# Optimization experiments

Hardware: AMD Instinct MI355X
Metric: run time of the kernel (lower is better)

## Reference

```python
import jax, jax.numpy as jnp
import numpy as np

EPS = 1e-5
THRESH = 1.5


def _compute_one(x, g_w, g_b, phi_w, phi_b, W_w, W_b, gamma, beta):
    # x: (c, w, h, z) -- single sample (torch code calls compute_x with batch 1)
    c, w, h, z = x.shape
    nz = z // 2
    # AdaptiveAvgPool3d(1) on x.permute(0,4,2,3,1): mean over (w, h, c) per z-slice -> (z,)
    p = x.mean(axis=(0, 1, 2))
    xp = x * p[None, None, None, :]
    # 1x1x1 conv projections (note: self.theta is defined but unused in the original)
    g_x = jnp.einsum('ic,cwhz->iwhz', g_w, x) + g_b[:, None, None, None]
    phi_x = jnp.einsum('ic,cwhz->iwhz', phi_w, xp) + phi_b[:, None, None, None]
    # MaxPool3d kernel (1,1,2): non-overlapping max pairs along z
    g_x = g_x.reshape(-1, w, h, nz, 2).max(axis=-1)      # (ic, w, h, nz)
    phi_x = phi_x.reshape(-1, w, h, nz, 2).max(axis=-1)  # (ic, w, h, nz)
    # theta_x: (x*p).permute(0,2,3,4,1).view(w*h, z, c)
    theta = xp.transpose(1, 2, 3, 0).reshape(w * h, z, c)
    # phi: permute(0,2,3,1,4).view(w*h, ic, nz)
    phi_m = phi_x.transpose(1, 2, 0, 3).reshape(w * h, -1, nz)
    # g: permute(0,2,3,4,1).view(w*h, nz, ic)
    g_m = g_x.transpose(1, 2, 3, 0).reshape(w * h, nz, -1)
    f = jnp.einsum('bzc,bcn->bzn', theta, phi_m)          # (wh, z, nz)
    a = jax.nn.softmax(f, axis=-1)
    y = jnp.einsum('bzn,bni->bzi', a, g_m)                # (wh, z, ic)
    y = y.reshape(w, h, z, -1).transpose(3, 0, 1, 2)      # (ic, w, h, z)
    wy = jnp.einsum('ci,iwhz->cwhz', W_w, y) + W_b[:, None, None, None]
    # BatchNorm3d in training mode on a single-sample batch: per-channel stats over (w,h,z)
    mu = wy.mean(axis=(1, 2, 3), keepdims=True)
    var = wy.var(axis=(1, 2, 3), keepdims=True)
    wy = (wy - mu) * jax.lax.rsqrt(var + EPS)
    wy = wy * gamma[:, None, None, None] + beta[:, None, None, None]
    return wy + x


def setup_inputs() -> dict:
    key = jax.random.key(0)
    ks = jax.random.split(key, 10)
    b, c, w, h, z = 2, 64, 64, 64, 64
    ic = c  # inter_channels defaults to in_channels
    x = jax.random.normal(ks[0], (b, c, w, h, z), dtype=jnp.float32)
    # spacings in [0, 3): some samples fall above spacing_thresh=1.5 (identity branch)
    spacings = jax.random.uniform(ks[1], (b, 3), dtype=jnp.float32) * 3.0
    g_w = jax.random.normal(ks[2], (ic, c), dtype=jnp.float32) * 0.1
    g_b = jax.random.normal(ks[3], (ic,), dtype=jnp.float32) * 0.1
    phi_w = jax.random.normal(ks[4], (ic, c), dtype=jnp.float32) * 0.1
    phi_b = jax.random.normal(ks[5], (ic,), dtype=jnp.float32) * 0.1
    W_w = jax.random.normal(ks[6], (c, ic), dtype=jnp.float32) * 0.1
    W_b = jax.random.normal(ks[7], (c,), dtype=jnp.float32) * 0.1
    gamma = jax.random.normal(ks[8], (c,), dtype=jnp.float32) * 0.1
    beta = jax.random.normal(ks[9], (c,), dtype=jnp.float32) * 0.1
    return {"x": x, "spacings": spacings, "g_w": g_w, "g_b": g_b,
            "phi_w": phi_w, "phi_b": phi_b, "W_w": W_w, "W_b": W_b,
            "gamma": gamma, "beta": beta}


def reference(x, spacings, g_w, g_b, phi_w, phi_b, W_w, W_b, gamma, beta):
    out = jax.vmap(_compute_one, in_axes=(0,) + (None,) * 8)(
        x, g_w, g_b, phi_w, phi_b, W_w, W_b, gamma, beta)
    use = (spacings[:, -1] <= THRESH)[:, None, None, None, None]
    return jnp.where(use, out, x)
```

## Files before the change

kernel.cpp:

```cpp
#include <hip/hip_runtime.h>
#include <hip/hip_bf16.h>
#include <math.h>

#define THRESH_SP 1.5f
#define WHZc   262144
#define CWHZc  16777216

#define WS_PSUM   0
#define WS_SLOT   128
#define WS_ZERO_N 8320
#define WS_W16_BYTE  65536
#define WS_WY_BYTE   131072
#define WS_W16_NEED  (WS_W16_BYTE + 3u*4096u*2u)
#define WS_WY_NEED   (WS_WY_BYTE + 2u*CWHZc*2u)

typedef __attribute__((ext_vector_type(8))) short bf16x8;
typedef __attribute__((ext_vector_type(4))) float floatx4;
typedef __attribute__((ext_vector_type(4))) float f32x4;
typedef __attribute__((ext_vector_type(2))) unsigned int u32x2;

#define MFMA(a, b, c) __builtin_amdgcn_mfma_f32_16x16x32_bf16((a), (b), (c), 0, 0, 0)

__device__ __forceinline__ unsigned short f2b(float f) {
    __hip_bfloat16 h = __float2bfloat16(f);
    return __builtin_bit_cast(unsigned short, h);
}
__device__ __forceinline__ float b2f(unsigned short h) {
    unsigned int u = ((unsigned int)h) << 16;
    return __builtin_bit_cast(float, u);
}
__device__ __forceinline__ bf16x8 ldfrag(const unsigned short* p, int elem_off) {
    return *(const bf16x8*)(p + elem_off);
}

__global__ __launch_bounds__(256) void k_prep(const float* __restrict__ gw,
                                              const float* __restrict__ pw,
                                              const float* __restrict__ Ww,
                                              float* __restrict__ ws,
                                              unsigned short* __restrict__ w16,
                                              int usew16) {
    const int i = blockIdx.x * 256 + threadIdx.x;
    if (i < WS_ZERO_N) ws[i] = 0.0f;
    if (usew16 && i < 4096) {
        w16[i]        = f2b(gw[i]);
        w16[4096 + i] = f2b(pw[i]);
        w16[8192 + i] = f2b(Ww[i]);
    }
}

__global__ __launch_bounds__(256) void k_pmean(const float* __restrict__ x,
                                               const float* __restrict__ sp,
                                               float* __restrict__ ws) {
    const int b = blockIdx.x >> 9;
    if (sp[b*3 + 2] > THRESH_SP) return;
    const int jb = blockIdx.x & 511;
    __shared__ float s[64];
    const int t = threadIdx.x;
    if (t < 64) s[t] = 0.0f;
    __syncthreads();
    const int idx4 = jb * 256 + t;
    const int z0 = (idx4 & 15) * 4;
    float a0 = 0.f, a1 = 0.f, a2 = 0.f, a3 = 0.f;
    const float* xb = x + (size_t)b * CWHZc;
#pragma unroll 4
    for (int it = 0; it < 32; ++it) {
        const float4 v = *(const float4*)&xb[(size_t)(idx4 + it * 131072) * 4];
        a0 += v.x; a1 += v.y; a2 += v.z; a3 += v.w;
    }
    a0 += __shfl_xor(a0, 16); a0 += __shfl_xor(a0, 32);
    a1 += __shfl_xor(a1, 16); a1 += __shfl_xor(a1, 32);
    a2 += __shfl_xor(a2, 16); a2 += __shfl_xor(a2, 32);
    a3 += __shfl_xor(a3, 16); a3 += __shfl_xor(a3, 32);
    if ((t & 63) < 16) {
        unsafeAtomicAdd(&s[z0 + 0], a0);
        unsafeAtomicAdd(&s[z0 + 1], a1);
        unsafeAtomicAdd(&s[z0 + 2], a2);
        unsafeAtomicAdd(&s[z0 + 3], a3);
    }
    __syncthreads();
    if (t < 64) unsafeAtomicAdd(&ws[WS_PSUM + b * 64 + t], s[t]);
}

#define L_WG     0
#define L_WP     9216
#define L_XA     18432
#define L_GPA    27648
#define L_PHA    32768
#define L_XB     37376
#define L_GPB    46592
#define L_PHB    51712
#define L_ATB    56320
#define L_BIAS   61440
#define L_PS     62208
#define L_TOTAL  62464

__global__ __launch_bounds__(512, 4) void k_main(
    const float* __restrict__ x, const float* __restrict__ sp,
    const float* __restrict__ gw, const float* __restrict__ gb,
    const float* __restrict__ pw, const float* __restrict__ pb,
    const float* __restrict__ Wwp, const float* __restrict__ Wbp,
    float* __restrict__ out, unsigned short* __restrict__ wy16, int use16,
    const unsigned short* __restrict__ w16, int usew16,
    float* __restrict__ ws) {
    const int blk = blockIdx.x;
    const int b = blk >> 11;
    if (sp[b*3 + 2] > THRESH_SP) return;
    const int whpair = (blk & 2047) * 2;

    __shared__ char smem[L_TOTAL];
    unsigned short* wg   = (unsigned short*)(smem + L_WG);
    unsigned short* wp   = (unsigned short*)(smem + L_WP);
    float*          bias = (float*)(smem + L_BIAS);
    float*          p_s  = (float*)(smem + L_PS);
    float*          statsf = (float*)(smem + L_PHA);

    const int t   = threadIdx.x;
    const int wv  = t >> 6;
    const int cid = wv >> 2;
    const int tt  = t & 255;
    const int l   = t & 63;
    const int lr  = l & 15;
    const int lq  = l >> 4;
    const int zt  = (wv & 3) << 4;

    unsigned short* xT   = (unsigned short*)(smem + (cid ? L_XB  : L_XA));
    unsigned short* gpT  = (unsigned short*)(smem + (cid ? L_GPB : L_GPA));
    unsigned short* phpN = (unsigned short*)(smem + (cid ? L_PHB : L_PHA));
    unsigned short* aT   = (unsigned short*)(smem + (cid ? L_ATB : L_WG));

    const int wh    = whpair + cid;
    const int xbase = b * CWHZc + wh * 64;

    {
        const int pr = tt >> 3;
        const int zo = tt & 7;
        const int c0 = pr * 2;
        const float* xc = &x[xbase + c0 * WHZc];
        const float4 A0 = *(const float4*)&xc[zo * 4];
        const float4 A1 = *(const float4*)&xc[zo * 4 + 32];
        const float4 B0 = *(const float4*)&xc[WHZc + zo * 4];
        const float4 B1 = *(const float4*)&xc[WHZc + zo * 4 + 32];
#pragma unroll
        for (int g = 0; g < 2; ++g) {
            const float4 va = g ? A1 : A0;
            const float4 vb = g ? B1 : B0;
            const int zb = (zo + 8 * g) * 4;
            const float av[4] = {va.x, va.y, va.z, va.w};
            const float bw[4] = {vb.x, vb.y, vb.z, vb.w};
#pragma unroll
            for (int j = 0; j < 4; ++j) {
                const int z = zb + j;
                const int chunk = (c0 >> 3) ^ ((z >> 2) & 3);
                const unsigned int pk =
                    (unsigned)f2b(av[j]) | ((unsigned)f2b(bw[j]) << 16);
                *(unsigned int*)&xT[z * 72 + chunk * 8 + (c0 & 7)] = pk;
            }
        }
    }
    if (usew16) {
#pragma unroll
        for (int k = 0; k < 2; ++k) {
            const int f = t + (k << 9);
            const int mat = f >> 9;
            const int i = (f & 511) >> 3, seg = f & 7;
            unsigned short* dst = mat ? wp : wg;
            *(uint4*)&dst[i*72 + seg*8] = *(const uint4*)&w16[mat*4096 + i*64 + seg*8];
        }
    } else {
#pragma unroll
        for (int k = 0; k < 4; ++k) {
            const int f = t + (k << 9);
            const int mat = f >> 10, ff = f & 1023;
            const int i = ff >> 4, c4 = ff & 15;
            const float* src = mat ? pw : gw;
            unsigned short* dst = mat ? wp : wg;
            const float4 v = *(const float4*)&src[i*64 + c4*4];
            uint2 pk;
            pk.x = (unsigned)f2b(v.x) | ((unsigned)f2b(v.y) << 16);
            pk.y = (unsigned)f2b(v.z) | ((unsigned)f2b(v.w) << 16);
            *(uint2*)&dst[i*72 + c4*4] = pk;
        }
    }
    if (t < 192) bias[t] = (t < 64) ? gb[t] : (t < 128) ? pb[t - 64] : Wbp[t - 128];
    if (t < 64)  p_s[t] = ws[WS_PSUM + b*64 + t] * (1.0f / 262144.0f);
    __syncthreads();

    const int zrow  = zt + lr;
    const int abase = zrow * 72 + ((lq ^ ((zrow >> 2) & 3)) << 3);
    const bf16x8 a0 = ldfrag(xT, abase);
    const bf16x8 a1 = ldfrag(xT, abase + 32);
    const float pz0 = p_s[zt + lq*4 + 0], pz1 = p_s[zt + lq*4 + 1];
    const float pz2 = p_s[zt + lq*4 + 2], pz3 = p_s[zt + lq*4 + 3];

    {
        const int n0 = (zt >> 1) + lq*2;
#pragma unroll
        for (int ti = 0; ti < 4; ++ti) {
            const int i = ti*16 + lr;
            const float bv = bias[i];
            floatx4 acc = {bv, bv, bv, bv};
            acc = MFMA(a0, ldfrag(wg, i*72 + lq*8), acc);
            acc = MFMA(a1, ldfrag(wg, i*72 + lq*8 + 32), acc);
            unsigned int pk = (unsigned)f2b(fmaxf(acc[0], acc[1])) |
                              ((unsigned)f2b(fmaxf(acc[2], acc[3])) << 16);
            *(unsigned int*)&gpT[i*40 + n0] = pk;
        }
    }
    __syncthreads();

    {
        const int n0 = (zt >> 1) + lq*2;
#pragma unroll
        for (int ti = 0; ti < 4; ++ti) {
            const int i = ti*16 + lr;
            floatx4 acc = {0.f, 0.f, 0.f, 0.f};
            acc = MFMA(a0, ldfrag(wp, i*72 + lq*8), acc);
            acc = MFMA(a1, ldfrag(wp, i*72 + lq*8 + 32), acc);
            const float bv = bias[64 + i];
            const float v0 = fmaf(acc[0], pz0, bv), v1 = fmaf(acc[1], pz1, bv);
            const float v2 = fmaf(acc[2], pz2, bv), v3 = fmaf(acc[3], pz3, bv);
            phpN[n0*72 + i]       = f2b(fmaxf(v0, v1));
            phpN[(n0 + 1)*72 + i] = f2b(fmaxf(v2, v3));
        }
    }
    __syncthreads();

    {
        floatx4 f0 = {0.f, 0.f, 0.f, 0.f}, f1 = {0.f, 0.f, 0.f, 0.f};
        f0 = MFMA(a0, ldfrag(phpN, lr*72 + lq*8), f0);
        f0 = MFMA(a1, ldfrag(phpN, lr*72 + lq*8 + 32), f0);
        f1 = MFMA(a0, ldfrag(phpN, (16 + lr)*72 + lq*8), f1);
        f1 = MFMA(a1, ldfrag(phpN, (16 + lr)*72 + lq*8 + 32), f1);
        if (usew16) {
            const int i = t >> 3, seg = t & 7;
            *(uint4*)&wp[i*72 + seg*8] = *(const uint4*)&w16[8192 + i*64 + seg*8];
        } else {
#pragma unroll
            for (int k = 0; k < 2; ++k) {
                const int f = t + (k << 9);
                const int i = f >> 4, c4 = f & 15;
                const float4 v = *(const float4*)&Wwp[i*64 + c4*4];
                uint2 pk;
                pk.x = (unsigned)f2b(v.x) | ((unsigned)f2b(v.y) << 16);
                pk.y = (unsigned)f2b(v.z) | ((unsigned)f2b(v.w) << 16);
                *(uint2*)&wp[i*72 + c4*4] = pk;
            }
        }
        const float pz[4] = {pz0, pz1, pz2, pz3};
#pragma unroll
        for (int r = 0; r < 4; ++r) {
            const float fr0 = f0[r] * pz[r], fr1 = f1[r] * pz[r];
            float m = fmaxf(fr0, fr1);
            m = fmaxf(m, __shfl_xor(m, 1)); m = fmaxf(m, __shfl_xor(m, 2));
            m = fmaxf(m, __shfl_xor(m, 4)); m = fmaxf(m, __shfl_xor(m, 8));
            const float e0 = __expf(fr0 - m), e1 = __expf(fr1 - m);
            float s = e0 + e1;
            s += __shfl_xor(s, 1); s += __shfl_xor(s, 2);
            s += __shfl_xor(s, 4); s += __shfl_xor(s, 8);
            const float inv = 1.0f / s;
            const int z = zt + lq*4 + r;
            aT[z*40 + lr]      = f2b(e0 * inv);
            aT[z*40 + lr + 16] = f2b(e1 * inv);
        }
    }
    __syncthreads();

    {
        if (t < 128) statsf[t] = 0.0f;
        const bf16x8 bv = ldfrag(aT, (zt + lr)*40 + lq*8);
        const int zcol = zt + lr;
        const int xzc = (zcol >> 2) & 3;
#pragma unroll
        for (int it = 0; it < 4; ++it) {
            const bf16x8 av = ldfrag(gpT, (it*16 + lr)*40 + lq*8);
            floatx4 acc = {0.f, 0.f, 0.f, 0.f};
            acc = MFMA(av, bv, acc);
            const int i0 = it*16 + lq*4;
            const int chunk = (i0 >> 3) ^ xzc;
            uint2 pk;
            pk.x = (unsigned)f2b(acc[0]) | ((unsigned)f2b(acc[1]) << 16);
            pk.y = (unsigned)f2b(acc[2]) | ((unsigned)f2b(acc[3]) << 16);
            *(uint2*)&xT[zcol*72 + chunk*8 + (i0 & 7)] = pk;
        }
    }
    __syncthreads();

    {
        const bf16x8 y0 = ldfrag(xT, abase);
        const bf16x8 y1 = ldfrag(xT, abase + 32);
#pragma unroll
        for (int ti = 0; ti < 4; ++ti) {
            const int co = ti*16 + lr;
            const float bv = bias[128 + co];
            floatx4 acc = {bv, bv, bv, bv};
            acc = MFMA(y0, ldfrag(wp, co*72 + lq*8), acc);
            acc = MFMA(y1, ldfrag(wp, co*72 + lq*8 + 32), acc);
            if (use16) {
                uint2 pk;
                pk.x = (unsigned)f2b(acc[0]) | ((unsigned)f2b(acc[1]) << 16);
                pk.y = (unsigned)f2b(acc[2]) | ((unsigned)f2b(acc[3]) << 16);
                *(uint2*)&wy16[(size_t)xbase + co * WHZc + zt + lq*4] = pk;
            } else {
                *(float4*)&out[xbase + co * WHZc + zt + lq*4] = *(float4*)&acc;
            }
            float s1 = acc[0] + acc[1] + acc[2] + acc[3];
            float s2 = acc[0]*acc[0] + acc[1]*acc[1] + acc[2]*acc[2] + acc[3]*acc[3];
            s1 += __shfl_xor(s1, 16); s1 += __shfl_xor(s1, 32);
            s2 += __shfl_xor(s2, 16); s2 += __shfl_xor(s2, 32);
            if (lq == 0) {
                atomicAdd(&statsf[co*2],     s1);
                atomicAdd(&statsf[co*2 + 1], s2);
            }
        }
    }
    __syncthreads();
    if (t < 128) {
        const int slot = blk & 31;
        unsafeAtomicAdd(&ws[WS_SLOT + (slot*2 + b)*128 + t], statsf[t]);
    }
}

__global__ __launch_bounds__(256) void k_final(const float* __restrict__ x,
                                               const float* __restrict__ sp,
                                               const float* __restrict__ gamma,
                                               const float* __restrict__ beta,
                                               float* __restrict__ out,
                                               const unsigned short* __restrict__ wy16,
                                               int use16,
                                               const float* __restrict__ ws) {
    const bool use0 = sp[2] <= THRESH_SP;
    const bool use1 = sp[5] <= THRESH_SP;
    __shared__ float scf[128], shf[128];
    if ((use0 || use1) && threadIdx.x < 128) {
        const int t = threadIdx.x;
        const int b = t >> 6, c = t & 63;
        float S1 = 0.f, S2 = 0.f;
        for (int s = 0; s < 32; s++) {
            S1 += ws[WS_SLOT + (s*2 + b)*128 + c*2 + 0];
            S2 += ws[WS_SLOT + (s*2 + b)*128 + c*2 + 1];
        }
        const float N = 262144.0f;
        const float mu = S1 / N;
        const float var = fmaxf(S2 / N - mu * mu, 0.0f);
        const float sc = gamma[c] * rsqrtf(var + 1e-5f);
        scf[t] = sc;
        shf[t] = beta[c] - mu * sc;
    }
    __syncthreads();
    const int nf4 = (2 * CWHZc) / 4;
    for (int i4 = blockIdx.x * blockDim.x + threadIdx.x; i4 < nf4;
         i4 += gridDim.x * blockDim.x) {
        const int idx = i4 * 4;
        const int b = idx >> 24;
        const bool use = b ? use1 : use0;
        const f32x4 xv = __builtin_nontemporal_load((const f32x4*)&x[idx]);
        f32x4 ov;
        if (use) {
            const int c = (idx >> 18) & 63;
            const float scv = scf[b * 64 + c];
            const float shv = shf[b * 64 + c];
            float w0, w1, w2, w3;
            if (use16) {
                const u32x2 q = __builtin_nontemporal_load((const u32x2*)&wy16[idx]);
                w0 = b2f((unsigned short)(q.x & 0xffffu));
                w1 = b2f((unsigned short)(q.x >> 16));
                w2 = b2f((unsigned short)(q.y & 0xffffu));
                w3 = b2f((unsigned short)(q.y >> 16));
            } else {
                const float4 wy = *(const float4*)&out[idx];
                w0 = wy.x; w1 = wy.y; w2 = wy.z; w3 = wy.w;
            }
            ov.x = w0 * scv + shv + xv.x;
            ov.y = w1 * scv + shv + xv.y;
            ov.z = w2 * scv + shv + xv.z;
            ov.w = w3 * scv + shv + xv.w;
        } else {
            ov = xv;
        }
        __builtin_nontemporal_store(ov, (f32x4*)&out[idx]);
    }
}

extern "C" void kernel_launch(void* const* d_in, const int* in_sizes, int n_in,
                              void* d_out, int out_size, void* d_ws, size_t ws_size,
                              hipStream_t stream) {
    const float* x     = (const float*)d_in[0];
    const float* spv   = (const float*)d_in[1];
    const float* gw    = (const float*)d_in[2];
    const float* gb    = (const float*)d_in[3];
    const float* pw    = (const float*)d_in[4];
    const float* pb    = (const float*)d_in[5];
    const float* Ww    = (const float*)d_in[6];
    const float* Wb    = (const float*)d_in[7];
    const float* gamma = (const float*)d_in[8];
    const float* beta  = (const float*)d_in[9];
    float* out = (float*)d_out;
    float* ws  = (float*)d_ws;
    const int usew16 = (ws_size >= (size_t)WS_W16_NEED) ? 1 : 0;
    const int use16  = (ws_size >= (size_t)WS_WY_NEED) ? 1 : 0;
    unsigned short* w16  = (unsigned short*)((char*)d_ws + WS_W16_BYTE);
    unsigned short* wy16 = (unsigned short*)((char*)d_ws + WS_WY_BYTE);

    k_prep<<<48, 256, 0, stream>>>(gw, pw, Ww, ws, w16, usew16);
    k_pmean<<<1024, 256, 0, stream>>>(x, spv, ws);
    k_main<<<4096, 512, 0, stream>>>(x, spv, gw, gb, pw, pb, Ww, Wb,
                                     out, wy16, use16, w16, usew16, ws);
    k_final<<<2048, 256, 0, stream>>>(x, spv, gamma, beta, out, wy16, use16, ws);
}
```

Baseline: 129.3 us.

## Keep phi and W weights in registers, fuse g/phi projections, drop LDS syncs

The phi and W weight fragments now stay in registers instead of LDS. This shrinks shared memory per block and lets the g and phi projections run in one loop, which removes two __syncthreads barriers. The prep kernel becomes a hipMemsetAsync plus one extra block in the mean kernel, and p is read directly from global memory. The trade-off is higher register pressure at 512 threads with launch_bounds 4, and possible LDS hazards now that those barriers are gone.

```diff
diff --git a/kernel.cpp b/kernel.cpp
--- a/kernel.cpp
+++ b/kernel.cpp
@@ -32,30 +32,37 @@
 __device__ __forceinline__ bf16x8 ldfrag(const unsigned short* p, int elem_off) {
     return *(const bf16x8*)(p + elem_off);
 }
-
-__global__ __launch_bounds__(256) void k_prep(const float* __restrict__ gw,
-                                              const float* __restrict__ pw,
-                                              const float* __restrict__ Ww,
-                                              float* __restrict__ ws,
-                                              unsigned short* __restrict__ w16,
-                                              int usew16) {
-    const int i = blockIdx.x * 256 + threadIdx.x;
-    if (i < WS_ZERO_N) ws[i] = 0.0f;
-    if (usew16 && i < 4096) {
-        w16[i]        = f2b(gw[i]);
-        w16[4096 + i] = f2b(pw[i]);
-        w16[8192 + i] = f2b(Ww[i]);
-    }
+__device__ __forceinline__ bf16x8 cvt8(const float* p) {
+    bf16x8 r;
+#pragma unroll
+    for (int j = 0; j < 8; ++j) r[j] = (short)f2b(p[j]);
+    return r;
 }
 
 __global__ __launch_bounds__(256) void k_pmean(const float* __restrict__ x,
                                                const float* __restrict__ sp,
+                                               const float* __restrict__ gw,
+                                               const float* __restrict__ pw,
+                                               const float* __restrict__ Ww,
+                                               unsigned short* __restrict__ w16,
+                                               int usew16,
                                                float* __restrict__ ws) {
-    const int b = blockIdx.x >> 9;
+    const int blk = blockIdx.x;
+    const int t = threadIdx.x;
+    if (blk == 1024) {
+        if (usew16) {
+            for (int j = t; j < 4096; j += 256) {
+                w16[j]        = f2b(gw[j]);
+                w16[4096 + j] = f2b(pw[j]);
+                w16[8192 + j] = f2b(Ww[j]);
+            }
+        }
+        return;
+    }
+    const int b = blk >> 9;
     if (sp[b*3 + 2] > THRESH_SP) return;
-    const int jb = blockIdx.x & 511;
+    const int jb = blk & 511;
     __shared__ float s[64];
-    const int t = threadIdx.x;
     if (t < 64) s[t] = 0.0f;
     __syncthreads();
     const int idx4 = jb * 256 + t;
@@ -82,17 +89,15 @@
 }
 
 #define L_WG     0
-#define L_WP     9216
-#define L_XA     18432
-#define L_GPA    27648
-#define L_PHA    32768
-#define L_XB     37376
-#define L_GPB    46592
-#define L_PHB    51712
-#define L_ATB    56320
-#define L_BIAS   61440
-#define L_PS     62208
-#define L_TOTAL  62464
+#define L_XA     9216
+#define L_GPA    18432
+#define L_PHA    23552
+#define L_XB     28160
+#define L_GPB    37376
+#define L_PHB    42496
+#define L_ATB    47104
+#define L_BIAS   52224
+#define L_TOTAL  52992
 
 __global__ __launch_bounds__(512, 4) void k_main(
     const float* __restrict__ x, const float* __restrict__ sp,
@@ -108,11 +113,9 @@
     const int whpair = (blk & 2047) * 2;
 
     __shared__ char smem[L_TOTAL];
+    __shared__ float statsf[128];
     unsigned short* wg   = (unsigned short*)(smem + L_WG);
-    unsigned short* wp   = (unsigned short*)(smem + L_WP);
     float*          bias = (float*)(smem + L_BIAS);
-    float*          p_s  = (float*)(smem + L_PS);
-    float*          statsf = (float*)(smem + L_PHA);
 
     const int t   = threadIdx.x;
     const int wv  = t >> 6;
@@ -130,6 +133,23 @@
 
     const int wh    = whpair + cid;
     const int xbase = b * CWHZc + wh * 64;
+
+    bf16x8 wf[8];
+    if (usew16) {
+#pragma unroll
+        for (int ti = 0; ti < 4; ++ti) {
+            const int i = ti*16 + lr;
+            wf[ti*2]     = *(const bf16x8*)(w16 + 4096 + i*64 + lq*8);
+            wf[ti*2 + 1] = *(const bf16x8*)(w16 + 4096 + i*64 + lq*8 + 32);
+        }
+    } else {
+#pragma unroll
+        for (int ti = 0; ti < 4; ++ti) {
+            const int i = ti*16 + lr;
+            wf[ti*2]     = cvt8(&pw[i*64 + lq*8]);
+            wf[ti*2 + 1] = cvt8(&pw[i*64 + lq*8 + 32]);
+        }
+    }
 
     {
         const int pr = tt >> 3;
@@ -158,69 +178,70 @@
         }
     }
     if (usew16) {
+        const int i = t >> 3, seg = t & 7;
+        *(uint4*)&wg[i*72 + seg*8] = *(const uint4*)&w16[i*64 + seg*8];
+    } else {
 #pragma unroll
         for (int k = 0; k < 2; ++k) {
             const int f = t + (k << 9);
-            const int mat = f >> 9;
-            const int i = (f & 511) >> 3, seg = f & 7;
-            unsigned short* dst = mat ? wp : wg;
-            *(uint4*)&dst[i*72 + seg*8] = *(const uint4*)&w16[mat*4096 + i*64 + seg*8];
-        }
-    } else {
-#pragma unroll
-        for (int k = 0; k < 4; ++k) {
-            const int f = t + (k << 9);
-            const int mat = f >> 10, ff = f & 1023;
-            const int i = ff >> 4, c4 = ff & 15;
-            const float* src = mat ? pw : gw;
-            unsigned short* dst = mat ? wp : wg;
-            const float4 v = *(const float4*)&src[i*64 + c4*4];
+            const int i = f >> 4, c4 = f & 15;
+            const float4 v = *(const float4*)&gw[i*64 + c4*4];
             uint2 pk;
             pk.x = (unsigned)f2b(v.x) | ((unsigned)f2b(v.y) << 16);
             pk.y = (unsigned)f2b(v.z) | ((unsigned)f2b(v.w) << 16);
-            *(uint2*)&dst[i*72 + c4*4] = pk;
+            *(uint2*)&wg[i*72 + c4*4] = pk;
         }
     }
     if (t < 192) bias[t] = (t < 64) ? gb[t] : (t < 128) ? pb[t - 64] : Wbp[t - 128];
-    if (t < 64)  p_s[t] = ws[WS_PSUM + b*64 + t] * (1.0f / 262144.0f);
+    if (t < 128) statsf[t] = 0.0f;
     __syncthreads();
 
     const int zrow  = zt + lr;
     const int abase = zrow * 72 + ((lq ^ ((zrow >> 2) & 3)) << 3);
     const bf16x8 a0 = ldfrag(xT, abase);
     const bf16x8 a1 = ldfrag(xT, abase + 32);
-    const float pz0 = p_s[zt + lq*4 + 0], pz1 = p_s[zt + lq*4 + 1];
-    const float pz2 = p_s[zt + lq*4 + 2], pz3 = p_s[zt + lq*4 + 3];
+    const float pinv = 1.0f / 262144.0f;
+    const float pz0 = ws[WS_PSUM + b*64 + zt + lq*4 + 0] * pinv;
+    const float pz1 = ws[WS_PSUM + b*64 + zt + lq*4 + 1] * pinv;
+    const float pz2 = ws[WS_PSUM + b*64 + zt + lq*4 + 2] * pinv;
+    const float pz3 = ws[WS_PSUM + b*64 + zt + lq*4 + 3] * pinv;
 
     {
         const int n0 = (zt >> 1) + lq*2;
 #pragma unroll
         for (int ti = 0; ti < 4; ++ti) {
             const int i = ti*16 + lr;
-            const float bv = bias[i];
-            floatx4 acc = {bv, bv, bv, bv};
-            acc = MFMA(a0, ldfrag(wg, i*72 + lq*8), acc);
-            acc = MFMA(a1, ldfrag(wg, i*72 + lq*8 + 32), acc);
-            unsigned int pk = (unsigned)f2b(fmaxf(acc[0], acc[1])) |
-                              ((unsigned)f2b(fmaxf(acc[2], acc[3])) << 16);
+            const float gbv = bias[i];
+            floatx4 accg = {gbv, gbv, gbv, gbv};
+            accg = MFMA(a0, ldfrag(wg, i*72 + lq*8), accg);
+            accg = MFMA(a1, ldfrag(wg, i*72 + lq*8 + 32), accg);
+            unsigned int pk = (unsigned)f2b(fmaxf(accg[0], accg[1])) |
+                              ((unsigned)f2b(fmaxf(accg[2], accg[3])) << 16);
             *(unsigned int*)&gpT[i*40 + n0] = pk;
-        }
-    }
-    __syncthreads();
-
-    {
-        const int n0 = (zt >> 1) + lq*2;
-#pragma unroll
-        for (int ti = 0; ti < 4; ++ti) {
-            const int i = ti*16 + lr;
-            floatx4 acc = {0.f, 0.f, 0.f, 0.f};
-            acc = MFMA(a0, ldfrag(wp, i*72 + lq*8), acc);
-            acc = MFMA(a1, ldfrag(wp, i*72 + lq*8 + 32), acc);
-            const float bv = bias[64 + i];
-            const float v0 = fmaf(acc[0], pz0, bv), v1 = fmaf(acc[1], pz1, bv);
-            const float v2 = fmaf(acc[2], pz2, bv), v3 = fmaf(acc[3], pz3, bv);
+
+            floatx4 accp = {0.f, 0.f, 0.f, 0.f};
+            accp = MFMA(a0, wf[ti*2], accp);
+            accp = MFMA(a1, wf[ti*2 + 1], accp);
+            const float pbv = bias[64 + i];
+            const float v0 = fmaf(accp[0], pz0, pbv), v1 = fmaf(accp[1], pz1, pbv);
+            const float v2 = fmaf(accp[2], pz2, pbv), v3 = fmaf(accp[3], pz3, pbv);
             phpN[n0*72 + i]       = f2b(fmaxf(v0, v1));
             phpN[(n0 + 1)*72 + i] = f2b(fmaxf(v2, v3));
+        }
+    }
+    if (usew16) {
+#pragma unroll
+        for (int ti = 0; ti < 4; ++ti) {
+            const int i = ti*16 + lr;
+            wf[ti*2]     = *(const bf16x8*)(w16 + 8192 + i*64 + lq*8);
+            wf[ti*2 + 1] = *(const bf16x8*)(w16 + 8192 + i*64 + lq*8 + 32);
+        }
+    } else {
+#pragma unroll
+        for (int ti = 0; ti < 4; ++ti) {
+            const int i = ti*16 + lr;
+            wf[ti*2]     = cvt8(&Wwp[i*64 + lq*8]);
+            wf[ti*2 + 1] = cvt8(&Wwp[i*64 + lq*8 + 32]);
         }
     }
     __syncthreads();
@@ -231,21 +252,6 @@
         f0 = MFMA(a1, ldfrag(phpN, lr*72 + lq*8 + 32), f0);
         f1 = MFMA(a0, ldfrag(phpN, (16 + lr)*72 + lq*8), f1);
         f1 = MFMA(a1, ldfrag(phpN, (16 + lr)*72 + lq*8 + 32), f1);
-        if (usew16) {
-            const int i = t >> 3, seg = t & 7;
-            *(uint4*)&wp[i*72 + seg*8] = *(const uint4*)&w16[8192 + i*64 + seg*8];
-        } else {
-#pragma unroll
-            for (int k = 0; k < 2; ++k) {
-                const int f = t + (k << 9);
-                const int i = f >> 4, c4 = f & 15;
-                const float4 v = *(const float4*)&Wwp[i*64 + c4*4];
-                uint2 pk;
-                pk.x = (unsigned)f2b(v.x) | ((unsigned)f2b(v.y) << 16);
-                pk.y = (unsigned)f2b(v.z) | ((unsigned)f2b(v.w) << 16);
-                *(uint2*)&wp[i*72 + c4*4] = pk;
-            }
-        }
         const float pz[4] = {pz0, pz1, pz2, pz3};
 #pragma unroll
         for (int r = 0; r < 4; ++r) {
@@ -263,10 +269,8 @@
             aT[z*40 + lr + 16] = f2b(e1 * inv);
         }
     }
-    __syncthreads();
 
     {
-        if (t < 128) statsf[t] = 0.0f;
         const bf16x8 bv = ldfrag(aT, (zt + lr)*40 + lq*8);
         const int zcol = zt + lr;
         const int xzc = (zcol >> 2) & 3;
@@ -283,7 +287,6 @@
             *(uint2*)&xT[zcol*72 + chunk*8 + (i0 & 7)] = pk;
         }
     }
-    __syncthreads();
 
     {
         const bf16x8 y0 = ldfrag(xT, abase);
@@ -293,8 +296,8 @@
             const int co = ti*16 + lr;
             const float bv = bias[128 + co];
             floatx4 acc = {bv, bv, bv, bv};
-            acc = MFMA(y0, ldfrag(wp, co*72 + lq*8), acc);
-            acc = MFMA(y1, ldfrag(wp, co*72 + lq*8 + 32), acc);
+            acc = MFMA(y0, wf[ti*2], acc);
+            acc = MFMA(y1, wf[ti*2 + 1], acc);
             if (use16) {
                 uint2 pk;
                 pk.x = (unsigned)f2b(acc[0]) | ((unsigned)f2b(acc[1]) << 16);
@@ -401,8 +404,8 @@
     unsigned short* w16  = (unsigned short*)((char*)d_ws + WS_W16_BYTE);
     unsigned short* wy16 = (unsigned short*)((char*)d_ws + WS_WY_BYTE);
 
-    k_prep<<<48, 256, 0, stream>>>(gw, pw, Ww, ws, w16, usew16);
-    k_pmean<<<1024, 256, 0, stream>>>(x, spv, ws);
+    hipMemsetAsync(ws, 0, (size_t)WS_ZERO_N * sizeof(float), stream);
+    k_pmean<<<1025, 256, 0, stream>>>(x, spv, gw, pw, Ww, w16, usew16, ws);
     k_main<<<4096, 512, 0, stream>>>(x, spv, gw, gb, pw, pb, Ww, Wb,
                                      out, wy16, use16, w16, usew16, ws);
     k_final<<<2048, 256, 0, stream>>>(x, spv, gamma, beta, out, wy16, use16, ws);
```

After: 134.6 us. 1.04x slower.

## Fuse pmean, main and final passes into one cooperative persistent kernel

Applied to the files above, without the earlier changes.

Adds a cooperative kernel of 512 blocks that computes the per-z means, runs the attention and projection stages over 16 spatial positions per block, and then applies batch-norm plus the residual. Grid-wide syncs replace the kernel boundaries, which removes two launches and lets the final pass reread x while it may still be cached. The intermediate wy buffer is laid out per spatial position so stores are contiguous, and the phi tile pitch changes to 88. The cost is less parallelism than the 4096-block main kernel and the overhead of the grid syncs. The old three-kernel path stays as a fallback if the cooperative launch fails.

```diff
diff --git a/kernel.cpp b/kernel.cpp
--- a/kernel.cpp
+++ b/kernel.cpp
@@ -1,6 +1,9 @@
 #include <hip/hip_runtime.h>
+#include <hip/hip_cooperative_groups.h>
 #include <hip/hip_bf16.h>
 #include <math.h>
+
+namespace cg = cooperative_groups;
 
 #define THRESH_SP 1.5f
 #define WHZc   262144
@@ -48,6 +51,334 @@
     }
 }
 
+#define F_WG    0
+#define F_WP    9216
+#define F_XA    18432
+#define F_XB    27648
+#define F_GPA   36864
+#define F_GPB   41984
+#define F_PA    47104
+#define F_PB    52736
+#define F_BIAS  58368
+#define F_TOTAL 59136
+
+__global__ __launch_bounds__(512, 4) void k_fused(
+    const float* __restrict__ x, const float* __restrict__ sp,
+    const float* __restrict__ gw, const float* __restrict__ gb,
+    const float* __restrict__ pw, const float* __restrict__ pb,
+    const float* __restrict__ Wwp, const float* __restrict__ Wbp,
+    const float* __restrict__ gamma, const float* __restrict__ beta,
+    float* __restrict__ out, unsigned short* __restrict__ wy16, int use16,
+    const unsigned short* __restrict__ w16, int usew16,
+    float* __restrict__ ws) {
+    const int blk = blockIdx.x;
+    const int t   = threadIdx.x;
+    const int b   = blk >> 8;
+    const bool useMe = sp[b*3 + 2] <= THRESH_SP;
+
+    __shared__ char smem[F_TOTAL];
+    __shared__ float statsf[128];
+    unsigned short* wg   = (unsigned short*)(smem + F_WG);
+    unsigned short* wp   = (unsigned short*)(smem + F_WP);
+    float*          bias = (float*)(smem + F_BIAS);
+
+    const int wv  = t >> 6;
+    const int cid = wv >> 2;
+    const int tt  = t & 255;
+    const int l   = t & 63;
+    const int lr  = l & 15;
+    const int lq  = l >> 4;
+    const int zt  = (wv & 3) << 4;
+
+    unsigned short* xT   = (unsigned short*)(smem + (cid ? F_XB  : F_XA));
+    unsigned short* gpT  = (unsigned short*)(smem + (cid ? F_GPB : F_GPA));
+    unsigned short* phpN = (unsigned short*)(smem + (cid ? F_PB : F_PA));
+    unsigned short* aT   = phpN;
+
+    const int whbase = (blk & 255) * 16;
+
+    if (useMe) {
+        if (t < 64) statsf[t] = 0.0f;
+        __syncthreads();
+        const int j4 = t & 255;
+        const int z0 = (j4 & 15) * 4;
+        const size_t pbase = (size_t)b * CWHZc + whbase * 64;
+        float a0 = 0.f, a1 = 0.f, a2 = 0.f, a3 = 0.f;
+#pragma unroll 4
+        for (int it = 0; it < 32; ++it) {
+            const int c = it * 2 + (t >> 8);
+            const float4 v = *(const float4*)&x[pbase + (size_t)c * WHZc + j4 * 4];
+            a0 += v.x; a1 += v.y; a2 += v.z; a3 += v.w;
+        }
+        a0 += __shfl_xor(a0, 16); a0 += __shfl_xor(a0, 32);
+        a1 += __shfl_xor(a1, 16); a1 += __shfl_xor(a1, 32);
+        a2 += __shfl_xor(a2, 16); a2 += __shfl_xor(a2, 32);
+        a3 += __shfl_xor(a3, 16); a3 += __shfl_xor(a3, 32);
+        if ((t & 63) < 16) {
+            atomicAdd(&statsf[z0 + 0], a0);
+            atomicAdd(&statsf[z0 + 1], a1);
+            atomicAdd(&statsf[z0 + 2], a2);
+            atomicAdd(&statsf[z0 + 3], a3);
+        }
+        __syncthreads();
+        if (t < 64) unsafeAtomicAdd(&ws[WS_PSUM + b * 64 + t], statsf[t]);
+    }
+    cg::this_grid().sync();
+
+    if (useMe) {
+        if (usew16) {
+            const int i = t >> 3, seg = t & 7;
+            *(uint4*)&wg[i*72 + seg*8] = *(const uint4*)&w16[i*64 + seg*8];
+        } else {
+#pragma unroll
+            for (int k = 0; k < 2; ++k) {
+                const int f = t + (k << 9);
+                const int i = f >> 4, c4 = f & 15;
+                const float4 v = *(const float4*)&gw[i*64 + c4*4];
+                uint2 pk;
+                pk.x = (unsigned)f2b(v.x) | ((unsigned)f2b(v.y) << 16);
+                pk.y = (unsigned)f2b(v.z) | ((unsigned)f2b(v.w) << 16);
+                *(uint2*)&wg[i*72 + c4*4] = pk;
+            }
+        }
+        if (t < 192) bias[t] = (t < 64) ? gb[t] : (t < 128) ? pb[t-64] : Wbp[t-128];
+        if (t < 128) statsf[t] = 0.0f;
+        const float pinv = 1.0f / 262144.0f;
+        const float pz0 = ws[WS_PSUM + b*64 + zt + lq*4 + 0] * pinv;
+        const float pz1 = ws[WS_PSUM + b*64 + zt + lq*4 + 1] * pinv;
+        const float pz2 = ws[WS_PSUM + b*64 + zt + lq*4 + 2] * pinv;
+        const float pz3 = ws[WS_PSUM + b*64 + zt + lq*4 + 3] * pinv;
+
+        for (int pair = 0; pair < 8; ++pair) {
+            __syncthreads();
+            const int wh    = whbase + pair*2 + cid;
+            const int xbase = b * CWHZc + wh * 64;
+
+            {
+                const int pr = tt >> 3, zo = tt & 7;
+                const int c0 = pr * 2;
+                const float* xc = &x[xbase + c0 * WHZc];
+                const float4 A0 = *(const float4*)&xc[zo * 4];
+                const float4 A1 = *(const float4*)&xc[zo * 4 + 32];
+                const float4 B0 = *(const float4*)&xc[WHZc + zo * 4];
+                const float4 B1 = *(const float4*)&xc[WHZc + zo * 4 + 32];
+#pragma unroll
+                for (int g = 0; g < 2; ++g) {
+                    const float4 va = g ? A1 : A0;
+                    const float4 vb = g ? B1 : B0;
+                    const int zb = (zo + 8 * g) * 4;
+                    const float av[4] = {va.x, va.y, va.z, va.w};
+                    const float bw[4] = {vb.x, vb.y, vb.z, vb.w};
+#pragma unroll
+                    for (int j = 0; j < 4; ++j) {
+                        const int z = zb + j;
+                        const int chunk = (c0 >> 3) ^ ((z >> 2) & 3);
+                        const unsigned int pk =
+                            (unsigned)f2b(av[j]) | ((unsigned)f2b(bw[j]) << 16);
+                        *(unsigned int*)&xT[z * 72 + chunk * 8 + (c0 & 7)] = pk;
+                    }
+                }
+            }
+            if (usew16) {
+                const int i = t >> 3, seg = t & 7;
+                *(uint4*)&wp[i*72 + seg*8] = *(const uint4*)&w16[4096 + i*64 + seg*8];
+            } else {
+#pragma unroll
+                for (int k = 0; k < 2; ++k) {
+                    const int f = t + (k << 9);
+                    const int i = f >> 4, c4 = f & 15;
+                    const float4 v = *(const float4*)&pw[i*64 + c4*4];
+                    uint2 pk;
+                    pk.x = (unsigned)f2b(v.x) | ((unsigned)f2b(v.y) << 16);
+                    pk.y = (unsigned)f2b(v.z) | ((unsigned)f2b(v.w) << 16);
+                    *(uint2*)&wp[i*72 + c4*4] = pk;
+                }
+            }
+            __syncthreads();
+
+            const int zrow  = zt + lr;
+            const int abase = zrow * 72 + ((lq ^ ((zrow >> 2) & 3)) << 3);
+            const bf16x8 a0 = ldfrag(xT, abase);
+            const bf16x8 a1 = ldfrag(xT, abase + 32);
+
+            {
+                const int n0 = (zt >> 1) + lq*2;
+#pragma unroll
+                for (int ti = 0; ti < 4; ++ti) {
+                    const int i = ti*16 + lr;
+                    const float bv = bias[i];
+                    floatx4 acc = {bv, bv, bv, bv};
+                    acc = MFMA(a0, ldfrag(wg, i*72 + lq*8), acc);
+                    acc = MFMA(a1, ldfrag(wg, i*72 + lq*8 + 32), acc);
+                    unsigned int pk = (unsigned)f2b(fmaxf(acc[0], acc[1])) |
+                                      ((unsigned)f2b(fmaxf(acc[2], acc[3])) << 16);
+                    *(unsigned int*)&gpT[i*40 + n0] = pk;
+                }
+#pragma unroll
+                for (int ti = 0; ti < 4; ++ti) {
+                    const int i = ti*16 + lr;
+                    floatx4 acc = {0.f, 0.f, 0.f, 0.f};
+                    acc = MFMA(a0, ldfrag(wp, i*72 + lq*8), acc);
+                    acc = MFMA(a1, ldfrag(wp, i*72 + lq*8 + 32), acc);
+                    const float bv = bias[64 + i];
+                    const float v0 = fmaf(acc[0], pz0, bv), v1 = fmaf(acc[1], pz1, bv);
+                    const float v2 = fmaf(acc[2], pz2, bv), v3 = fmaf(acc[3], pz3, bv);
+                    phpN[n0*88 + i]       = f2b(fmaxf(v0, v1));
+                    phpN[(n0 + 1)*88 + i] = f2b(fmaxf(v2, v3));
+                }
+            }
+            __syncthreads();
+
+            floatx4 f0 = {0.f, 0.f, 0.f, 0.f}, f1 = {0.f, 0.f, 0.f, 0.f};
+            f0 = MFMA(a0, ldfrag(phpN, lr*88 + lq*8), f0);
+            f0 = MFMA(a1, ldfrag(phpN, lr*88 + lq*8 + 32), f0);
+            f1 = MFMA(a0, ldfrag(phpN, (16 + lr)*88 + lq*8), f1);
+            f1 = MFMA(a1, ldfrag(phpN, (16 + lr)*88 + lq*8 + 32), f1);
+            if (usew16) {
+                const int i = t >> 3, seg = t & 7;
+                *(uint4*)&wp[i*72 + seg*8] = *(const uint4*)&w16[8192 + i*64 + seg*8];
+            } else {
+#pragma unroll
+                for (int k = 0; k < 2; ++k) {
+                    const int f = t + (k << 9);
+                    const int i = f >> 4, c4 = f & 15;
+                    const float4 v = *(const float4*)&Wwp[i*64 + c4*4];
+                    uint2 pk;
+                    pk.x = (unsigned)f2b(v.x) | ((unsigned)f2b(v.y) << 16);
+                    pk.y = (unsigned)f2b(v.z) | ((unsigned)f2b(v.w) << 16);
+                    *(uint2*)&wp[i*72 + c4*4] = pk;
+                }
+            }
+            __syncthreads();
+
+            {
+                const float pz[4] = {pz0, pz1, pz2, pz3};
+#pragma unroll
+                for (int r = 0; r < 4; ++r) {
+                    const float fr0 = f0[r] * pz[r], fr1 = f1[r] * pz[r];
+                    float m = fmaxf(fr0, fr1);
+                    m = fmaxf(m, __shfl_xor(m, 1)); m = fmaxf(m, __shfl_xor(m, 2));
+                    m = fmaxf(m, __shfl_xor(m, 4)); m = fmaxf(m, __shfl_xor(m, 8));
+                    const float e0 = __expf(fr0 - m), e1 = __expf(fr1 - m);
+                    float s = e0 + e1;
+                    s += __shfl_xor(s, 1); s += __shfl_xor(s, 2);
+                    s += __shfl_xor(s, 4); s += __shfl_xor(s, 8);
+                    const float inv = 1.0f / s;
+                    const int z = zt + lq*4 + r;
+                    aT[z*40 + lr]      = f2b(e0 * inv);
+                    aT[z*40 + lr + 16] = f2b(e1 * inv);
+                }
+            }
+
+            {
+                const bf16x8 bv = ldfrag(aT, (zt + lr)*40 + lq*8);
+                const int zcol = zt + lr;
+                const int xzc = (zcol >> 2) & 3;
+#pragma unroll
+                for (int it = 0; it < 4; ++it) {
+                    const bf16x8 av = ldfrag(gpT, (it*16 + lr)*40 + lq*8);
+                    floatx4 acc = {0.f, 0.f, 0.f, 0.f};
+                    acc = MFMA(av, bv, acc);
+                    const int i0 = it*16 + lq*4;
+                    const int chunk = (i0 >> 3) ^ xzc;
+                    uint2 pk;
+                    pk.x = (unsigned)f2b(acc[0]) | ((unsigned)f2b(acc[1]) << 16);
+                    pk.y = (unsigned)f2b(acc[2]) | ((unsigned)f2b(acc[3]) << 16);
+                    *(uint2*)&xT[zcol*72 + chunk*8 + (i0 & 7)] = pk;
+                }
+            }
+
+            {
+                const bf16x8 y0 = ldfrag(xT, abase);
+                const bf16x8 y1 = ldfrag(xT, abase + 32);
+                const int bwh = b * 4096 + wh;
+#pragma unroll
+                for (int ti = 0; ti < 4; ++ti) {
+                    const int co = ti*16 + lr;
+                    const float bv = bias[128 + co];
+                    floatx4 acc = {bv, bv, bv, bv};
+                    acc = MFMA(y0, ldfrag(wp, co*72 + lq*8), acc);
+                    acc = MFMA(y1, ldfrag(wp, co*72 + lq*8 + 32), acc);
+                    if (use16) {
+                        uint2 pk;
+                        pk.x = (unsigned)f2b(acc[0]) | ((unsigned)f2b(acc[1]) << 16);
+                        pk.y = (unsigned)f2b(acc[2]) | ((unsigned)f2b(acc[3]) << 16);
+                        *(uint2*)&wy16[((size_t)bwh << 12) + (co << 6) + zt + lq*4] = pk;
+                    } else {
+                        *(float4*)&out[xbase + co * WHZc + zt + lq*4] = *(float4*)&acc;
+                    }
+                    float s1 = acc[0] + acc[1] + acc[2] + acc[3];
+                    float s2 = acc[0]*acc[0] + acc[1]*acc[1] + acc[2]*acc[2] + acc[3]*acc[3];
+                    s1 += __shfl_xor(s1, 16); s1 += __shfl_xor(s1, 32);
+                    s2 += __shfl_xor(s2, 16); s2 += __shfl_xor(s2, 32);
+                    if (lq == 0) {
+                        atomicAdd(&statsf[co*2],     s1);
+                        atomicAdd(&statsf[co*2 + 1], s2);
+                    }
+                }
+            }
+        }
+        __syncthreads();
+        if (t < 128) {
+            const int slot = blk & 31;
+            unsafeAtomicAdd(&ws[WS_SLOT + (slot*2 + b)*128 + t], statsf[t]);
+        }
+    }
+    cg::this_grid().sync();
+
+    float* scsh = (float*)smem;
+    if (useMe && t < 64) {
+        float S1 = 0.f, S2 = 0.f;
+        for (int s = 0; s < 32; s++) {
+            S1 += ws[WS_SLOT + (s*2 + b)*128 + t*2 + 0];
+            S2 += ws[WS_SLOT + (s*2 + b)*128 + t*2 + 1];
+        }
+        const float N = 262144.0f;
+        const float mu = S1 / N;
+        const float var = fmaxf(S2 / N - mu * mu, 0.0f);
+        const float sc = gamma[t] * rsqrtf(var + 1e-5f);
+        scsh[t]      = sc;
+        scsh[64 + t] = beta[t] - mu * sc;
+    }
+    __syncthreads();
+#pragma unroll 2
+    for (int j = 0; j < 16; ++j) {
+        const int wh = whbase + j;
+        const size_t base = (size_t)b * CWHZc + wh * 64;
+#pragma unroll
+        for (int r = 0; r < 2; ++r) {
+            const int item = t + r*512;
+            const int co = item >> 4, z4 = item & 15;
+            const size_t idx = base + (size_t)co * WHZc + z4 * 4;
+            const f32x4 xv = *(const f32x4*)&x[idx];
+            f32x4 ov;
+            if (useMe) {
+                const float scv = scsh[co];
+                const float shv = scsh[64 + co];
+                float w0, w1, w2, w3;
+                if (use16) {
+                    const size_t widx = ((size_t)(b*4096 + wh) << 12) + (co << 6) + z4*4;
+                    const u32x2 q = *(const u32x2*)&wy16[widx];
+                    w0 = b2f((unsigned short)(q.x & 0xffffu));
+                    w1 = b2f((unsigned short)(q.x >> 16));
+                    w2 = b2f((unsigned short)(q.y & 0xffffu));
+                    w3 = b2f((unsigned short)(q.y >> 16));
+                } else {
+                    const float4 wy = *(const float4*)&out[idx];
+                    w0 = wy.x; w1 = wy.y; w2 = wy.z; w3 = wy.w;
+                }
+                ov.x = w0 * scv + shv + xv.x;
+                ov.y = w1 * scv + shv + xv.y;
+                ov.z = w2 * scv + shv + xv.z;
+                ov.w = w3 * scv + shv + xv.w;
+            } else {
+                ov = xv;
+            }
+            __builtin_nontemporal_store(ov, (f32x4*)&out[idx]);
+        }
+    }
+}
+
 __global__ __launch_bounds__(256) void k_pmean(const float* __restrict__ x,
                                                const float* __restrict__ sp,
                                                float* __restrict__ ws) {
@@ -132,8 +463,7 @@
     const int xbase = b * CWHZc + wh * 64;
 
     {
-        const int pr = tt >> 3;
-        const int zo = tt & 7;
+        const int pr = tt >> 3, zo = tt & 7;
         const int c0 = pr * 2;
         const float* xc = &x[xbase + c0 * WHZc];
         const float4 A0 = *(const float4*)&xc[zo * 4];
@@ -207,7 +537,6 @@
         }
     }
     __syncthreads();
-
     {
         const int n0 = (zt >> 1) + lq*2;
 #pragma unroll
@@ -224,7 +553,6 @@
         }
     }
     __syncthreads();
-
     {
         floatx4 f0 = {0.f, 0.f, 0.f, 0.f}, f1 = {0.f, 0.f, 0.f, 0.f};
         f0 = MFMA(a0, ldfrag(phpN, lr*72 + lq*8), f0);
@@ -264,7 +592,6 @@
         }
     }
     __syncthreads();
-
     {
         if (t < 128) statsf[t] = 0.0f;
         const bf16x8 bv = ldfrag(aT, (zt + lr)*40 + lq*8);
@@ -284,7 +611,6 @@
         }
     }
     __syncthreads();
-
     {
         const bf16x8 y0 = ldfrag(xT, abase);
         const bf16x8 y1 = ldfrag(xT, abase + 32);
@@ -396,14 +722,25 @@
     const float* beta  = (const float*)d_in[9];
     float* out = (float*)d_out;
     float* ws  = (float*)d_ws;
-    const int usew16 = (ws_size >= (size_t)WS_W16_NEED) ? 1 : 0;
-    const int use16  = (ws_size >= (size_t)WS_WY_NEED) ? 1 : 0;
+    int usew16 = (ws_size >= (size_t)WS_W16_NEED) ? 1 : 0;
+    int use16  = (ws_size >= (size_t)WS_WY_NEED) ? 1 : 0;
     unsigned short* w16  = (unsigned short*)((char*)d_ws + WS_W16_BYTE);
     unsigned short* wy16 = (unsigned short*)((char*)d_ws + WS_WY_BYTE);
 
     k_prep<<<48, 256, 0, stream>>>(gw, pw, Ww, ws, w16, usew16);
-    k_pmean<<<1024, 256, 0, stream>>>(x, spv, ws);
-    k_main<<<4096, 512, 0, stream>>>(x, spv, gw, gb, pw, pb, Ww, Wb,
-                                     out, wy16, use16, w16, usew16, ws);
-    k_final<<<2048, 256, 0, stream>>>(x, spv, gamma, beta, out, wy16, use16, ws);
-}
+
+    void* args[] = {
+        (void*)&x, (void*)&spv, (void*)&gw, (void*)&gb, (void*)&pw, (void*)&pb,
+        (void*)&Ww, (void*)&Wb, (void*)&gamma, (void*)&beta,
+        (void*)&out, (void*)&wy16, (void*)&use16,
+        (void*)&w16, (void*)&usew16, (void*)&ws
+    };
+    hipError_t err = hipLaunchCooperativeKernel((void*)k_fused, dim3(512), dim3(512),
+                                                args, 0, stream);
+    if (err != hipSuccess) {
+        k_pmean<<<1024, 256, 0, stream>>>(x, spv, ws);
+        k_main<<<4096, 512, 0, stream>>>(x, spv, gw, gb, pw, pb, Ww, Wb,
+                                         out, wy16, use16, w16, usew16, ws);
+        k_final<<<2048, 256, 0, stream>>>(x, spv, gamma, beta, out, wy16, use16, ws);
+    }
+}
```

Result: slower. 205.4 us (+58.8%).
